# Performance work log

Hardware: AMD Instinct MI355X
Metric: run time of the kernel (lower is better)

## Reference

```python
import jax, jax.numpy as jnp
import numpy as np

NEG_SLOPE = 0.2  # PyG GATConv default negative_slope
N_NODES = 50000


def gat_conv(x, src, dst, W, att_src, att_dst, bias, heads, out_ch):
    # x: [N, F_in]; src/dst: [E] (messages flow src -> dst, softmax over dst)
    N = x.shape[0]
    h = (x @ W).reshape(N, heads, out_ch)              # [N,H,C]
    a_src = jnp.sum(h * att_src, axis=-1)              # [N,H]
    a_dst = jnp.sum(h * att_dst, axis=-1)              # [N,H]
    e = jax.nn.leaky_relu(a_src[src] + a_dst[dst], NEG_SLOPE)   # [E,H]
    # numerically stable segment softmax over incoming edges of each dst node
    m = jax.ops.segment_max(e, dst, num_segments=N)    # [N,H]
    e = jnp.exp(e - m[dst])
    denom = jax.ops.segment_sum(e, dst, num_segments=N)
    alpha = e / (denom[dst] + 1e-16)                   # [E,H]
    msg = h[src] * alpha[:, :, None]                   # [E,H,C]
    out = jax.ops.segment_sum(msg, dst, num_segments=N)  # [N,H,C]
    return out.reshape(N, heads * out_ch) + bias


def add_self_loops(edge_index, num_nodes):
    loop = jnp.arange(num_nodes, dtype=edge_index.dtype)
    return jnp.concatenate([edge_index, jnp.stack([loop, loop])], axis=1)


def setup_inputs() -> dict:
    key = jax.random.key(0)
    ks = jax.random.split(key, 10)
    F_in, H, C, F_out = 256, 4, 64, 16
    x = jax.random.normal(ks[0], (N_NODES, F_in), dtype=jnp.float32)
    edge_index = jax.random.randint(ks[1], (2, 800000), 0, N_NODES, dtype=jnp.int64)
    s1 = 1.0 / np.sqrt(F_in)
    s2 = 1.0 / np.sqrt(H * C)
    return {
        "x": x,
        "edge_index": edge_index,
        "W1": jax.random.normal(ks[2], (F_in, H * C), dtype=jnp.float32) * s1,
        "att_src1": jax.random.normal(ks[3], (H, C), dtype=jnp.float32) * s2,
        "att_dst1": jax.random.normal(ks[4], (H, C), dtype=jnp.float32) * s2,
        "b1": jnp.zeros((H * C,), dtype=jnp.float32),
        "W2": jax.random.normal(ks[5], (H * C, F_out), dtype=jnp.float32) * s2,
        "att_src2": jax.random.normal(ks[6], (1, F_out), dtype=jnp.float32) * 0.25,
        "att_dst2": jax.random.normal(ks[7], (1, F_out), dtype=jnp.float32) * 0.25,
        "b2": jnp.zeros((F_out,), dtype=jnp.float32),
    }


def reference(x, edge_index, W1, att_src1, att_dst1, b1, W2, att_src2, att_dst2, b2):
    ei = add_self_loops(edge_index, x.shape[0])
    src, dst = ei[0], ei[1]
    H1, C1 = att_src1.shape
    h = gat_conv(x, src, dst, W1, att_src1, att_dst1, b1, H1, C1)
    h = jax.nn.relu(h)
    # F.dropout(training=False) is identity in eval mode
    H2, C2 = att_src2.shape
    out = gat_conv(h, src, dst, W2, att_src2, att_dst2, b2, H2, C2)
    return jax.nn.log_softmax(out, axis=1)
```

## Files before the change

### kernel.cpp

```cpp
#include <hip/hip_runtime.h>
#include <math.h>


typedef __attribute__((ext_vector_type(8))) short bf16x8;
typedef __attribute__((ext_vector_type(8))) unsigned short u16x8;
typedef __attribute__((ext_vector_type(4))) float f32x4;
typedef __attribute__((ext_vector_type(2))) float f32x2;

#define BCAP 1536

static __device__ inline unsigned short f2bf(float f) {
    unsigned u = __builtin_bit_cast(unsigned, f);
    unsigned r = (u + 0x7FFF + ((u >> 16) & 1)) >> 16;
    return (unsigned short)r;
}
static __device__ inline float bf2f(unsigned short u) {
    unsigned v = ((unsigned)u) << 16;
    return __builtin_bit_cast(float, v);
}
static __device__ inline float lrelu(float x) { return x > 0.f ? x : 0.2f * x; }

__global__ __launch_bounds__(256) void k_prep_w1t(const float* __restrict__ W1,
                                                  short* __restrict__ w1t,
                                                  int* __restrict__ fill_bkt,
                                                  int nbuk) {
    int idx = blockIdx.x * 256 + threadIdx.x;
    if (idx < nbuk) fill_bkt[idx] = 0;
    int n = idx >> 8, k = idx & 255;
    w1t[n * 256 + k] = (short)f2bf(W1[k * 256 + n]);
}

__global__ __launch_bounds__(256) void k_bucketize(const int* __restrict__ ei,
                                                   int* __restrict__ fill_bkt,
                                                   uint2* __restrict__ tmp,
                                                   int E0, int nbuk) {
    __shared__ int hist[1024];
    __shared__ int base[1024];
    const int t = threadIdx.x;
    const int e0 = blockIdx.x * 4096;
    for (int b = t; b < nbuk; b += 256) hist[b] = 0;
    __syncthreads();
    int ss[16], ds[16];
    int nm = 0;
#pragma unroll
    for (int k = 0; k < 16; ++k) {
        int e = e0 + t + k * 256;
        if (e < E0) {
            ss[nm] = ei[e];
            ds[nm] = ei[E0 + e];
            atomicAdd(&hist[ds[nm] >> 6], 1);
            ++nm;
        }
    }
    __syncthreads();
    for (int b = t; b < nbuk; b += 256) {
        int c = hist[b];
        base[b] = c ? atomicAdd(&fill_bkt[b], c) : 0;
        hist[b] = 0;
    }
    __syncthreads();
    for (int k = 0; k < nm; ++k) {
        int b = ds[k] >> 6;
        int r = base[b] + atomicAdd(&hist[b], 1);
        if (r < BCAP) tmp[(long)b * BCAP + r] = make_uint2((unsigned)ss[k], (unsigned)ds[k]);
    }
}

__global__ __launch_bounds__(256) void k_csr_fill(const uint2* __restrict__ tmp,
                                                  const int* __restrict__ fill_bkt,
                                                  int* __restrict__ off,
                                                  int* __restrict__ csr,
                                                  int N, int nbuk) {
    __shared__ int hist[64];
    __shared__ int loff[64];
    __shared__ int lfill[64];
    __shared__ int sbase;
    const int b = blockIdx.x;
    const int t = threadIdx.x;
    if (t < 64) { hist[t] = 0; lfill[t] = 0; }
    __syncthreads();
    int cnt = min(fill_bkt[b], BCAP);
    const uint2* tp = tmp + (long)b * BCAP;
    for (int i = t; i < cnt; i += 256)
        atomicAdd(&hist[tp[i].y & 63], 1);
    if (t >= 64 && t < 128) {
        int l = t - 64;
        int acc = 0;
        for (int i = l; i < b; i += 64) acc += min(fill_bkt[i], BCAP);
#pragma unroll
        for (int o = 1; o < 64; o <<= 1) acc += __shfl_xor(acc, o);
        if (l == 0) sbase = acc + 64 * b;
        if (b == nbuk - 1 && l == 0) {
            int tot = acc + 64 * b + min(fill_bkt[b], BCAP) + (N - b * 64);
            off[N] = tot;
        }
    }
    __syncthreads();
    if (t < 64) {
        int v = hist[t] + 1;
        int incl = v;
#pragma unroll
        for (int o = 1; o < 64; o <<= 1) {
            int u = __shfl_up(incl, o);
            if (t >= (unsigned)o) incl += u;
        }
        int lo = sbase + incl - v;
        loff[t] = lo;
        int d = b * 64 + t;
        if (d < N) off[d] = lo;
    }
    __syncthreads();
    for (int i = t; i < cnt; i += 256) {
        uint2 e = tp[i];
        int dl = e.y & 63;
        int r = atomicAdd(&lfill[dl], 1);
        csr[loff[dl] + r] = (int)e.x;
    }
    __syncthreads();
    if (t < 64) {
        int d = b * 64 + t;
        if (d < N) csr[loff[t] + hist[t]] = d;
    }
}

__global__ __launch_bounds__(256) void k_gemm1_mfma(const float* __restrict__ A,
                                                    const short* __restrict__ Bt,
                                                    const float* __restrict__ att_s,
                                                    const float* __restrict__ att_d,
                                                    unsigned char* __restrict__ C8,
                                                    float* __restrict__ a1s,
                                                    float* __restrict__ a1d,
                                                    int M) {
    __shared__ short As[128][40];
    __shared__ short Bs[128][40];
    const int bm = blockIdx.y * 128;
    const int bn = blockIdx.x * 128;
    const int tid = threadIdx.x;
    const int lane = tid & 63;
    const int wave = tid >> 6;
    const int wm = (wave >> 1) * 64;
    const int wn = (wave & 1) * 64;
    const int l15 = lane & 15;
    const int l4 = lane >> 4;

    const int sr = tid >> 1;
    const int sh = (tid & 1) * 16;

    f32x4 acc[4][4] = {};

    for (int k0 = 0; k0 < 256; k0 += 32) {
        {
            float v[16];
            if (bm + sr < M) {
                const float* p = &A[(long)(bm + sr) * 256 + k0 + sh];
#pragma unroll
                for (int q = 0; q < 4; ++q) {
                    float4 fv = *(const float4*)(p + q * 4);
                    v[q * 4 + 0] = fv.x; v[q * 4 + 1] = fv.y;
                    v[q * 4 + 2] = fv.z; v[q * 4 + 3] = fv.w;
                }
            } else {
#pragma unroll
                for (int q = 0; q < 16; ++q) v[q] = 0.f;
            }
            short b[16];
#pragma unroll
            for (int q = 0; q < 16; ++q) b[q] = (short)f2bf(v[q]);
            *(bf16x8*)&As[sr][sh] = *(bf16x8*)&b[0];
            *(bf16x8*)&As[sr][sh + 8] = *(bf16x8*)&b[8];
        }
        {
            const short* p = &Bt[(long)(bn + sr) * 256 + k0 + sh];
            bf16x8 b0 = *(const bf16x8*)p;
            bf16x8 b1 = *(const bf16x8*)(p + 8);
            *(bf16x8*)&Bs[sr][sh] = b0;
            *(bf16x8*)&Bs[sr][sh + 8] = b1;
        }
        __syncthreads();

        bf16x8 af[4], bfr[4];
#pragma unroll
        for (int i = 0; i < 4; ++i)
            af[i] = *(const bf16x8*)&As[wm + i * 16 + l15][l4 * 8];
#pragma unroll
        for (int j = 0; j < 4; ++j)
            bfr[j] = *(const bf16x8*)&Bs[wn + j * 16 + l15][l4 * 8];
#pragma unroll
        for (int i = 0; i < 4; ++i)
#pragma unroll
            for (int j = 0; j < 4; ++j)
                acc[i][j] = __builtin_amdgcn_mfma_f32_16x16x32_bf16(af[i], bfr[j], acc[i][j], 0, 0, 0);
        __syncthreads();
    }

    const int h = (bn + wn) >> 6;
    float aws[4], awd[4];
#pragma unroll
    for (int j = 0; j < 4; ++j) {
        aws[j] = att_s[h * 64 + j * 16 + l15];
        awd[j] = att_d[h * 64 + j * 16 + l15];
    }

#pragma unroll
    for (int i = 0; i < 4; ++i) {
#pragma unroll
        for (int r = 0; r < 4; ++r) {
            float sv = 0.f, dv = 0.f;
#pragma unroll
            for (int j = 0; j < 4; ++j) {
                sv += acc[i][j][r] * aws[j];
                dv += acc[i][j][r] * awd[j];
            }
#pragma unroll
            for (int o = 1; o < 16; o <<= 1) {
                sv += __shfl_xor(sv, o);
                dv += __shfl_xor(dv, o);
            }
            int row = bm + wm + i * 16 + l4 * 4 + r;
            if (row < M) {
                if (l15 == 0) { a1s[row * 4 + h] = sv; a1d[row * 4 + h] = dv; }
#pragma unroll
                for (int j = 0; j < 4; ++j) {
                    float vv = acc[i][j][r];
                    C8[(long)row * 256 + bn + wn + j * 16 + l15] =
                        (unsigned char)(__builtin_amdgcn_cvt_pk_fp8_f32(vv, vv, 0, false) & 0xFF);
                }
            }
        }
    }
}

__global__ __launch_bounds__(256) void k_gather1(const unsigned char* __restrict__ h1f8,
                                                 const int* __restrict__ off,
                                                 const int* __restrict__ csr,
                                                 const float* __restrict__ as1,
                                                 const float* __restrict__ ad1,
                                                 float* __restrict__ alphaE,
                                                 const float* __restrict__ b1,
                                                 unsigned short* __restrict__ out1b,
                                                 int N) {
    int wid = blockIdx.x * 4 + (threadIdx.x >> 6);
    int lane = threadIdx.x & 63;
    if (wid >= N) return;
    int begin = off[wid], end = off[wid + 1];

    float inv;
    {
        int h = lane >> 4, t = lane & 15;
        float adh = ad1[wid * 4 + h];
        float den = 0.f;
        for (int j = begin + t; j < end; j += 16) {
            float ex = __expf(lrelu(as1[csr[j] * 4 + h] + adh));
            alphaE[j * 4 + h] = ex;
            den += ex;
        }
#pragma unroll
        for (int o = 1; o < 16; o <<= 1) den += __shfl_xor(den, o);
        inv = 1.f / (den + 1e-16f);
    }
    __threadfence_block();

    const int es = lane >> 4;
    const int cl = lane & 15;
    const int hc = cl >> 2;
    const float inv_c = __shfl(inv, hc * 16);

    f32x2 acc2[8] = {};
#pragma unroll 2
    for (int j0 = begin; j0 < end; j0 += 4) {
        int j = j0 + es;
        bool valid = j < end;
        int jc = valid ? j : begin;
        int s = csr[jc];
        float a = valid ? alphaE[jc * 4 + hc] : 0.f;
        f32x2 av = {a, a};
        uint4 v = *(const uint4*)&h1f8[(long)s * 256 + cl * 16];
        unsigned w[4] = {v.x, v.y, v.z, v.w};
#pragma unroll
        for (int q = 0; q < 4; ++q) {
            f32x2 lo = __builtin_amdgcn_cvt_pk_f32_fp8((int)w[q], false);
            f32x2 hi = __builtin_amdgcn_cvt_pk_f32_fp8((int)w[q], true);
            acc2[q * 2 + 0] += av * lo;
            acc2[q * 2 + 1] += av * hi;
        }
    }
    float accf[16];
#pragma unroll
    for (int q = 0; q < 8; ++q) { accf[2 * q] = acc2[q].x; accf[2 * q + 1] = acc2[q].y; }
#pragma unroll
    for (int q = 0; q < 16; ++q) {
        accf[q] += __shfl_xor(accf[q], 16);
        accf[q] += __shfl_xor(accf[q], 32);
    }
    if (lane < 16) {
        unsigned pk[8];
#pragma unroll
        for (int q = 0; q < 8; ++q) {
            float v0 = fmaxf(accf[q * 2 + 0] * inv_c + b1[cl * 16 + q * 2 + 0], 0.f);
            float v1 = fmaxf(accf[q * 2 + 1] * inv_c + b1[cl * 16 + q * 2 + 1], 0.f);
            pk[q] = (unsigned)f2bf(v0) | ((unsigned)f2bf(v1) << 16);
        }
        unsigned short* dst = &out1b[(long)wid * 256 + cl * 16];
        *(uint4*)dst = make_uint4(pk[0], pk[1], pk[2], pk[3]);
        *(uint4*)(dst + 8) = make_uint4(pk[4], pk[5], pk[6], pk[7]);
    }
}

__global__ __launch_bounds__(256) void k_gemm2(const unsigned short* __restrict__ Xb,
                                               const float* __restrict__ W,
                                               const float* __restrict__ att_s,
                                               const float* __restrict__ att_d,
                                               float* __restrict__ h2,
                                               float* __restrict__ a2s,
                                               float* __restrict__ a2d, int N) {
    __shared__ float Ws[256 * 16];
    for (int i = threadIdx.x; i < 1024; i += 256)
        ((float4*)Ws)[i] = ((const float4*)W)[i];
    __syncthreads();
    int r = threadIdx.x >> 4, c = threadIdx.x & 15;
    int row = blockIdx.x * 16 + r;
    if (row >= N) return;
    const unsigned short* xr = Xb + (long)row * 256;
    float acc = 0.f;
    for (int k = 0; k < 256; k += 8) {
        u16x8 xv = *(const u16x8*)&xr[k];
#pragma unroll
        for (int q = 0; q < 8; ++q) acc += bf2f(xv[q]) * Ws[(k + q) * 16 + c];
    }
    h2[row * 16 + c] = acc;
    float vs = acc * att_s[c];
    float vd = acc * att_d[c];
    for (int o = 1; o < 16; o <<= 1) { vs += __shfl_xor(vs, o); vd += __shfl_xor(vd, o); }
    if (c == 0) { a2s[row] = vs; a2d[row] = vd; }
}

__global__ __launch_bounds__(256) void k_gather2(const float* __restrict__ h2,
                                                 const int* __restrict__ off,
                                                 const int* __restrict__ csr,
                                                 const float* __restrict__ a2s,
                                                 const float* __restrict__ a2d,
                                                 const float* __restrict__ b2,
                                                 float* __restrict__ out, int N) {
    int wid = blockIdx.x * 4 + (threadIdx.x >> 6);
    int lane = threadIdx.x & 63;
    if (wid >= N) return;
    int begin = off[wid], end = off[wid + 1];
    float adh = a2d[wid];
    float den = 0.f;
    for (int j = begin + lane; j < end; j += 64)
        den += __expf(lrelu(a2s[csr[j]] + adh));
#pragma unroll
    for (int o = 32; o; o >>= 1) den += __shfl_xor(den, o);
    float inv = 1.f / (den + 1e-16f);
    const int es = lane >> 4;
    const int c = lane & 15;
    float acc = 0.f;
#pragma unroll 2
    for (int j0 = begin; j0 < end; j0 += 4) {
        int j = j0 + es;
        bool valid = j < end;
        int jc = valid ? j : begin;
        int s = csr[jc];
        float a = valid ? __expf(lrelu(a2s[s] + adh)) : 0.f;
        acc += a * h2[(long)s * 16 + c];
    }
    acc += __shfl_xor(acc, 16);
    acc += __shfl_xor(acc, 32);
    float v = acc * inv + b2[c];
    float mx = v;
    for (int o = 1; o < 16; o <<= 1) mx = fmaxf(mx, __shfl_xor(mx, o));
    float se = __expf(v - mx);
    for (int o = 1; o < 16; o <<= 1) se += __shfl_xor(se, o);
    float r = v - mx - logf(se);
    if (lane < 16) out[(long)wid * 16 + c] = r;
}

extern "C" void kernel_launch(void* const* d_in, const int* in_sizes, int n_in,
                              void* d_out, int out_size, void* d_ws, size_t ws_size,
                              hipStream_t stream) {
    const float* x    = (const float*)d_in[0];
    const int*   ei   = (const int*)d_in[1];
    const float* W1   = (const float*)d_in[2];
    const float* as1w = (const float*)d_in[3];
    const float* ad1w = (const float*)d_in[4];
    const float* b1   = (const float*)d_in[5];
    const float* W2   = (const float*)d_in[6];
    const float* as2w = (const float*)d_in[7];
    const float* ad2w = (const float*)d_in[8];
    const float* b2   = (const float*)d_in[9];
    float* out = (float*)d_out;

    const int N    = in_sizes[0] / 256;
    const int E0   = in_sizes[1] / 2;
    const int Etot = E0 + N;
    const int NBUK = (N + 63) >> 6;

    char* p = (char*)d_ws;
    unsigned char*  h1f8  = (unsigned char*)p;  p += (size_t)N * 256;
    unsigned short* out1b = (unsigned short*)p; p += (size_t)N * 256 * sizeof(short);
    float* h2     = (float*)p; p += (size_t)N * 16 * sizeof(float);
    float* a1s    = (float*)p; p += (size_t)N * 4 * sizeof(float);
    float* a1d    = (float*)p; p += (size_t)N * 4 * sizeof(float);
    float* a2s    = (float*)p; p += (size_t)N * sizeof(float);
    float* a2d    = (float*)p; p += (size_t)N * sizeof(float);
    float* alphaE = (float*)p; p += (size_t)Etot * 4 * sizeof(float);
    int*   off    = (int*)p;   p += (size_t)(N + 1) * sizeof(int);
    int*   fillbk = (int*)p;   p += (size_t)NBUK * sizeof(int);
    short* w1t    = (short*)p; p += (size_t)256 * 256 * sizeof(short);
    int*   csr    = (int*)p;   p += (size_t)Etot * sizeof(int);
    uint2* tmp    = (uint2*)p; p += (size_t)NBUK * BCAP * sizeof(uint2);

    const int NW = (N + 3) / 4;

    hipLaunchKernelGGL(k_prep_w1t, dim3(256), dim3(256), 0, stream, W1, w1t, fillbk, NBUK);

    hipLaunchKernelGGL(k_bucketize, dim3((E0 + 4095) / 4096), dim3(256), 0, stream,
                       ei, fillbk, tmp, E0, NBUK);
    hipLaunchKernelGGL(k_csr_fill, dim3(NBUK), dim3(256), 0, stream,
                       tmp, fillbk, off, csr, N, NBUK);

    hipLaunchKernelGGL(k_gemm1_mfma, dim3(2, (N + 127) / 128), dim3(256), 0, stream,
                       x, w1t, as1w, ad1w, h1f8, a1s, a1d, N);
    hipLaunchKernelGGL(k_gather1, dim3(NW), dim3(256), 0, stream,
                       h1f8, off, csr, a1s, a1d, alphaE, b1, out1b, N);

    hipLaunchKernelGGL(k_gemm2, dim3((N + 15) / 16), dim3(256), 0, stream,
                       out1b, W2, as2w, ad2w, h2, a2s, a2d, N);
    hipLaunchKernelGGL(k_gather2, dim3(NW), dim3(256), 0, stream,
                       h2, off, csr, a2s, a2d, b2, out, N);
}
```

Measured before the change: 257.6 us.

## Pack fp8 h1 stores into dwords with permuted column layout; vectorize attention pass

The GEMM1 epilogue now packs four fp8 values into one 32-bit store per lane instead of four byte stores. This permutes the column order of h1, so gather1 reads a permuted bias and gemm2 remaps its weight indices to match. Gather1's softmax-denominator pass is also restructured to process one edge per lane across all four heads with float4 loads of a1s and alphaE. Byte-store traffic and scattered per-head loads should drop, at the cost of an implicit layout contract across three kernels.

```diff
diff --git a/kernel.cpp b/kernel.cpp
--- a/kernel.cpp
+++ b/kernel.cpp
@@ -20,12 +20,18 @@
 }
 static __device__ inline float lrelu(float x) { return x > 0.f ? x : 0.2f * x; }
 
-__global__ __launch_bounds__(256) void k_prep_w1t(const float* __restrict__ W1,
-                                                  short* __restrict__ w1t,
-                                                  int* __restrict__ fill_bkt,
-                                                  int nbuk) {
+__global__ __launch_bounds__(256) void k_prep(const float* __restrict__ W1,
+                                              const float* __restrict__ b1,
+                                              short* __restrict__ w1t,
+                                              float* __restrict__ b1p,
+                                              int* __restrict__ fill_bkt,
+                                              int nbuk) {
     int idx = blockIdx.x * 256 + threadIdx.x;
     if (idx < nbuk) fill_bkt[idx] = 0;
+    if (idx < 256) {
+        int ct = (idx >> 6) * 64 + (idx & 3) * 16 + ((idx & 63) >> 2);
+        b1p[idx] = b1[ct];
+    }
     int n = idx >> 8, k = idx & 255;
     w1t[n * 256 + k] = (short)f2bf(W1[k * 256 + n]);
 }
@@ -219,12 +225,10 @@
             int row = bm + wm + i * 16 + l4 * 4 + r;
             if (row < M) {
                 if (l15 == 0) { a1s[row * 4 + h] = sv; a1d[row * 4 + h] = dv; }
-#pragma unroll
-                for (int j = 0; j < 4; ++j) {
-                    float vv = acc[i][j][r];
-                    C8[(long)row * 256 + bn + wn + j * 16 + l15] =
-                        (unsigned char)(__builtin_amdgcn_cvt_pk_fp8_f32(vv, vv, 0, false) & 0xFF);
-                }
+                int d = 0;
+                d = __builtin_amdgcn_cvt_pk_fp8_f32(acc[i][0][r], acc[i][1][r], d, false);
+                d = __builtin_amdgcn_cvt_pk_fp8_f32(acc[i][2][r], acc[i][3][r], d, true);
+                *(unsigned*)&C8[(long)row * 256 + (bn + wn) + l15 * 4] = (unsigned)d;
             }
         }
     }
@@ -236,7 +240,7 @@
                                                  const float* __restrict__ as1,
                                                  const float* __restrict__ ad1,
                                                  float* __restrict__ alphaE,
-                                                 const float* __restrict__ b1,
+                                                 const float* __restrict__ b1p,
                                                  unsigned short* __restrict__ out1b,
                                                  int N) {
     int wid = blockIdx.x * 4 + (threadIdx.x >> 6);
@@ -244,26 +248,32 @@
     if (wid >= N) return;
     int begin = off[wid], end = off[wid + 1];
 
-    float inv;
-    {
-        int h = lane >> 4, t = lane & 15;
-        float adh = ad1[wid * 4 + h];
-        float den = 0.f;
-        for (int j = begin + t; j < end; j += 16) {
-            float ex = __expf(lrelu(as1[csr[j] * 4 + h] + adh));
-            alphaE[j * 4 + h] = ex;
-            den += ex;
-        }
-#pragma unroll
-        for (int o = 1; o < 16; o <<= 1) den += __shfl_xor(den, o);
-        inv = 1.f / (den + 1e-16f);
+    float4 ad4 = ((const float4*)ad1)[wid];
+    float den0 = 0.f, den1 = 0.f, den2 = 0.f, den3 = 0.f;
+    for (int j = begin + lane; j < end; j += 64) {
+        int s = csr[j];
+        float4 sc = ((const float4*)as1)[s];
+        float e0 = __expf(lrelu(sc.x + ad4.x));
+        float e1 = __expf(lrelu(sc.y + ad4.y));
+        float e2 = __expf(lrelu(sc.z + ad4.z));
+        float e3 = __expf(lrelu(sc.w + ad4.w));
+        ((float4*)alphaE)[j] = make_float4(e0, e1, e2, e3);
+        den0 += e0; den1 += e1; den2 += e2; den3 += e3;
+    }
+#pragma unroll
+    for (int o = 32; o; o >>= 1) {
+        den0 += __shfl_xor(den0, o);
+        den1 += __shfl_xor(den1, o);
+        den2 += __shfl_xor(den2, o);
+        den3 += __shfl_xor(den3, o);
     }
     __threadfence_block();
 
     const int es = lane >> 4;
     const int cl = lane & 15;
     const int hc = cl >> 2;
-    const float inv_c = __shfl(inv, hc * 16);
+    float denh = hc == 0 ? den0 : hc == 1 ? den1 : hc == 2 ? den2 : den3;
+    const float inv_c = 1.f / (denh + 1e-16f);
 
     f32x2 acc2[8] = {};
 #pragma unroll 2
@@ -296,8 +306,8 @@
         unsigned pk[8];
 #pragma unroll
         for (int q = 0; q < 8; ++q) {
-            float v0 = fmaxf(accf[q * 2 + 0] * inv_c + b1[cl * 16 + q * 2 + 0], 0.f);
-            float v1 = fmaxf(accf[q * 2 + 1] * inv_c + b1[cl * 16 + q * 2 + 1], 0.f);
+            float v0 = fmaxf(accf[q * 2 + 0] * inv_c + b1p[cl * 16 + q * 2 + 0], 0.f);
+            float v1 = fmaxf(accf[q * 2 + 1] * inv_c + b1p[cl * 16 + q * 2 + 1], 0.f);
             pk[q] = (unsigned)f2bf(v0) | ((unsigned)f2bf(v1) << 16);
         }
         unsigned short* dst = &out1b[(long)wid * 256 + cl * 16];
@@ -324,8 +334,12 @@
     float acc = 0.f;
     for (int k = 0; k < 256; k += 8) {
         u16x8 xv = *(const u16x8*)&xr[k];
-#pragma unroll
-        for (int q = 0; q < 8; ++q) acc += bf2f(xv[q]) * Ws[(k + q) * 16 + c];
+        int kb = (k >> 6) * 64 + ((k & 63) >> 2);
+#pragma unroll
+        for (int q = 0; q < 8; ++q) {
+            int ct = kb + (q & 3) * 16 + (q >> 2);
+            acc += bf2f(xv[q]) * Ws[ct * 16 + c];
+        }
     }
     h2[row * 16 + c] = acc;
     float vs = acc * att_s[c];
@@ -404,6 +418,7 @@
     float* a2s    = (float*)p; p += (size_t)N * sizeof(float);
     float* a2d    = (float*)p; p += (size_t)N * sizeof(float);
     float* alphaE = (float*)p; p += (size_t)Etot * 4 * sizeof(float);
+    float* b1p    = (float*)p; p += (size_t)256 * sizeof(float);
     int*   off    = (int*)p;   p += (size_t)(N + 1) * sizeof(int);
     int*   fillbk = (int*)p;   p += (size_t)NBUK * sizeof(int);
     short* w1t    = (short*)p; p += (size_t)256 * 256 * sizeof(short);
@@ -412,7 +427,7 @@
 
     const int NW = (N + 3) / 4;
 
-    hipLaunchKernelGGL(k_prep_w1t, dim3(256), dim3(256), 0, stream, W1, w1t, fillbk, NBUK);
+    hipLaunchKernelGGL(k_prep, dim3(256), dim3(256), 0, stream, W1, b1, w1t, b1p, fillbk, NBUK);
 
     hipLaunchKernelGGL(k_bucketize, dim3((E0 + 4095) / 4096), dim3(256), 0, stream,
                        ei, fillbk, tmp, E0, NBUK);
@@ -422,7 +437,7 @@
     hipLaunchKernelGGL(k_gemm1_mfma, dim3(2, (N + 127) / 128), dim3(256), 0, stream,
                        x, w1t, as1w, ad1w, h1f8, a1s, a1d, N);
     hipLaunchKernelGGL(k_gather1, dim3(NW), dim3(256), 0, stream,
-                       h1f8, off, csr, a1s, a1d, alphaE, b1, out1b, N);
+                       h1f8, off, csr, a1s, a1d, alphaE, b1p, out1b, N);
 
     hipLaunchKernelGGL(k_gemm2, dim3((N + 15) / 16), dim3(256), 0, stream,
                        out1b, W2, as2w, ad2w, h2, a2s, a2d, N);
```

Result: no change. 255.8 us (-0.7%).
